# Optimization experiments

Measured on AMD Instinct MI355X. Metric: run time of the kernel, lower is better.

## Reference

```python
import jax, jax.numpy as jnp
import numpy as np

N, IN_F, OUT_F, R = 8192, 4096, 4096, 16
ALPHA = 32
SCALING = ALPHA / R  # 2.0


def setup_inputs() -> dict:
    key = jax.random.key(0)
    k1, k2, k3, k4, k5 = jax.random.split(key, 5)
    return {
        "x": jax.random.normal(k1, (N, IN_F), dtype=jnp.float32),
        "W": jax.random.normal(k2, (OUT_F, IN_F), dtype=jnp.float32) * 0.02,
        "b": jax.random.normal(k3, (OUT_F,), dtype=jnp.float32) * 0.02,
        "lora_A": jax.random.normal(k4, (R, IN_F), dtype=jnp.float32) * 0.02,
        "lora_B": jax.random.normal(k5, (OUT_F, R), dtype=jnp.float32) * 0.02,
    }


def reference(x, W, b, lora_A, lora_B):
    # Base linear: x [N, in_f] @ W.T [in_f, out_f] + b -> [N, out_f]
    result = jnp.einsum('ni,oi->no', x, W) + b
    # LoRA path: (B @ (A @ x.T)).T * scaling == (x @ A.T) @ B.T * scaling
    lora = jnp.einsum('nr,or->no', jnp.einsum('ni,ri->nr', x, lora_A), lora_B)
    return result + lora * SCALING
```

## Files before the change

### kernel.cpp

```cpp
#include <hip/hip_runtime.h>
#include <hip/hip_bf16.h>
#include <stdint.h>

#define N_ROWS 8192
#define IN_F   4096
#define OUT_F  4096
#define R_LORA 16
#define KP     4160

typedef __bf16 bf16_t;
typedef __attribute__((ext_vector_type(8))) __bf16 bf16x8;
typedef __attribute__((ext_vector_type(4))) __bf16 bf16x4;
typedef __attribute__((ext_vector_type(4))) float  f32x4;
typedef __attribute__((ext_vector_type(16))) float f32x16;

__device__ __forceinline__ void load16_lds(const bf16_t* g, bf16_t* l) {
    auto gp = (const __attribute__((address_space(1))) void*)g;
    auto lp = (__attribute__((address_space(3))) void*)(uint32_t)(uintptr_t)l;
    __builtin_amdgcn_global_load_lds(gp, lp, 16, 0, 0);
}

#define PREPA_BLOCKS 2048

__global__ __launch_bounds__(256) void prep_fused(const float* __restrict__ x,
                                                  const float* __restrict__ W,
                                                  const float* __restrict__ bias,
                                                  const float* __restrict__ lA,
                                                  const float* __restrict__ lB,
                                                  bf16_t* __restrict__ Aw,
                                                  bf16_t* __restrict__ Bw) {
    int b = blockIdx.x;
    int t = threadIdx.x;
    if (b < PREPA_BLOCKS) {
        int row0 = b * 4;
        for (int rr = 0; rr < 4; ++rr) {
            int row = row0 + rr;
            const float4* xr = (const float4*)(x + (size_t)row * IN_F);
            bf16_t* ar = Aw + (size_t)row * KP;
            for (int s = t; s < 512; s += 256) {
                float4 f0 = xr[2 * s];
                float4 f1 = xr[2 * s + 1];
                bf16x8 v;
                v[0] = (bf16_t)f0.x; v[1] = (bf16_t)f0.y;
                v[2] = (bf16_t)f0.z; v[3] = (bf16_t)f0.w;
                v[4] = (bf16_t)f1.x; v[5] = (bf16_t)f1.y;
                v[6] = (bf16_t)f1.z; v[7] = (bf16_t)f1.w;
                *(bf16x8*)(ar + s * 8) = v;
            }
            if (t < 64) ar[IN_F + t] = (t == 0) ? (bf16_t)1.0f : (bf16_t)0.0f;
        }
    } else {
        int o0 = (b - PREPA_BLOCKS) * 4;
        float bl[4][R_LORA];
        for (int oo = 0; oo < 4; ++oo)
            for (int r = 0; r < R_LORA; ++r)
                bl[oo][r] = 2.0f * lB[(o0 + oo) * R_LORA + r];

        for (int j = 0; j < IN_F / (256 * 4); ++j) {
            int i4 = (j * 256 + t) * 4;
            f32x4 acc[4];
            for (int oo = 0; oo < 4; ++oo) {
                float4 w = *(const float4*)(W + (size_t)(o0 + oo) * IN_F + i4);
                acc[oo] = (f32x4){w.x, w.y, w.z, w.w};
            }
            for (int r = 0; r < R_LORA; ++r) {
                float4 a = *(const float4*)(lA + (size_t)r * IN_F + i4);
                for (int oo = 0; oo < 4; ++oo) {
                    acc[oo][0] += bl[oo][r] * a.x;
                    acc[oo][1] += bl[oo][r] * a.y;
                    acc[oo][2] += bl[oo][r] * a.z;
                    acc[oo][3] += bl[oo][r] * a.w;
                }
            }
            for (int oo = 0; oo < 4; ++oo) {
                bf16x4 v;
                v[0] = (bf16_t)acc[oo][0]; v[1] = (bf16_t)acc[oo][1];
                v[2] = (bf16_t)acc[oo][2]; v[3] = (bf16_t)acc[oo][3];
                *(bf16x4*)(Bw + (size_t)(o0 + oo) * KP + i4) = v;
            }
        }
        {
            int oo = t >> 6;
            int c  = IN_F + (t & 63);
            float v = (c == IN_F) ? bias[o0 + oo] : 0.0f;
            Bw[(size_t)(o0 + oo) * KP + c] = (bf16_t)v;
        }
    }
}

#define BM 256
#define BN 256
#define BK 64
#define NT (KP / BK)

__global__ __launch_bounds__(512, 2) void gemm_bt(const bf16_t* __restrict__ A,
                                                  const bf16_t* __restrict__ B,
                                                  float* __restrict__ C) {
    __shared__ __align__(16) bf16_t lds[2][2][BM * BK];

    int bid = blockIdx.x;
    int swz = (bid & 7) * 64 + (bid >> 3);
    int bm  = swz & 31;
    int bn  = swz >> 5;
    int rowBase = bm * BM;
    int colBase = bn * BN;

    const int t    = threadIdx.x;
    const int lane = t & 63;
    const int wave = t >> 6;
    const int l31  = lane & 31;
    const int lhi  = lane >> 5;
    const int l7   = lane & 7;
    const int wr   = wave >> 2;
    const int wc   = wave & 3;

    int rowOffA[4], colOffB[2];
#pragma unroll
    for (int rf = 0; rf < 4; ++rf) rowOffA[rf] = (wr * 128 + rf * 32 + l31) * BK;
#pragma unroll
    for (int cf = 0; cf < 2; ++cf) colOffB[cf] = (wc * 64 + cf * 32 + l31) * BK;

    uint32_t srcA[4], srcB[4];
#pragma unroll
    for (int s = 0; s < 4; ++s) {
        int c = s * 512 + t;
        int r = c >> 3, p = c & 7;
        uint32_t off = (uint32_t)(r * KP + ((p ^ (r & 7)) << 3));
        srcA[s] = (uint32_t)(rowBase * KP) + off;
        srcB[s] = (uint32_t)(colBase * KP) + off;
    }

    auto stage = [&](int bsel, int k0) {
#pragma unroll
        for (int s = 0; s < 4; ++s)
            load16_lds(A + srcA[s] + k0, &lds[bsel][0][(s * 512 + t) * 8]);
#pragma unroll
        for (int s = 0; s < 4; ++s)
            load16_lds(B + srcB[s] + k0, &lds[bsel][1][(s * 512 + t) * 8]);
    };

    f32x16 acc[4][2];
#pragma unroll
    for (int rf = 0; rf < 4; ++rf)
#pragma unroll
        for (int cf = 0; cf < 2; ++cf)
#pragma unroll
            for (int r = 0; r < 16; ++r) acc[rf][cf][r] = 0.f;

#define COMPUTE(bsel)                                                          \
    do {                                                                       \
        const bf16_t* Ab = &lds[bsel][0][0];                                   \
        const bf16_t* Bb = &lds[bsel][1][0];                                   \
        _Pragma("unroll")                                                      \
        for (int ks = 0; ks < 4; ++ks) {                                       \
            int pos = ((((ks << 1) | lhi)) ^ l7) << 3;                         \
            bf16x8 af[4], bf[2];                                               \
            _Pragma("unroll")                                                  \
            for (int rf = 0; rf < 4; ++rf)                                     \
                af[rf] = *(const bf16x8*)&Ab[rowOffA[rf] + pos];               \
            _Pragma("unroll")                                                  \
            for (int cf = 0; cf < 2; ++cf)                                     \
                bf[cf] = *(const bf16x8*)&Bb[colOffB[cf] + pos];               \
            __builtin_amdgcn_s_setprio(1);                                     \
            _Pragma("unroll")                                                  \
            for (int rf = 0; rf < 4; ++rf)                                     \
                _Pragma("unroll")                                              \
                for (int cf = 0; cf < 2; ++cf)                                 \
                    acc[rf][cf] = __builtin_amdgcn_mfma_f32_32x32x16_bf16(     \
                        af[rf], bf[cf], acc[rf][cf], 0, 0, 0);                 \
            __builtin_amdgcn_s_setprio(0);                                     \
        }                                                                      \
    } while (0)

    stage(0, 0);

    for (int kt = 0; kt < NT - 1; ++kt) {
        const int cur = kt & 1;
        const int nb  = cur ^ 1;
        __builtin_amdgcn_s_barrier();
        stage(nb, (kt + 1) * BK);
        asm volatile("s_waitcnt vmcnt(8)" ::: "memory");
        __builtin_amdgcn_s_barrier();
        COMPUTE(cur);
    }
    {
        __builtin_amdgcn_s_barrier();
        asm volatile("s_waitcnt vmcnt(0)" ::: "memory");
        __builtin_amdgcn_s_barrier();
        COMPUTE(0);
    }
#undef COMPUTE

#pragma unroll
    for (int rf = 0; rf < 4; ++rf) {
        int rB = rowBase + wr * 128 + rf * 32 + 4 * lhi;
#pragma unroll
        for (int cf = 0; cf < 2; ++cf) {
            int col = colBase + wc * 64 + cf * 32 + l31;
#pragma unroll
            for (int reg = 0; reg < 16; ++reg) {
                int row = rB + (reg & 3) + 8 * (reg >> 2);
                C[(size_t)row * OUT_F + col] = acc[rf][cf][reg];
            }
        }
    }
}

extern "C" void kernel_launch(void* const* d_in, const int* in_sizes, int n_in,
                              void* d_out, int out_size, void* d_ws, size_t ws_size,
                              hipStream_t stream) {
    const float* x  = (const float*)d_in[0];
    const float* W  = (const float*)d_in[1];
    const float* b  = (const float*)d_in[2];
    const float* lA = (const float*)d_in[3];
    const float* lB = (const float*)d_in[4];
    float* out = (float*)d_out;

    bf16_t* Aw = (bf16_t*)d_ws;
    bf16_t* Bw = Aw + (size_t)N_ROWS * KP;

    prep_fused<<<PREPA_BLOCKS + OUT_F / 4, 256, 0, stream>>>(x, W, b, lA, lB, Aw, Bw);
    gemm_bt<<<(N_ROWS / BM) * (OUT_F / BN), 512, 0, stream>>>(Aw, Bw, out);
}
```

Baseline: 538.9 us.

## Restructure GEMM inner loop into quadrant-wise LDS reads interleaved with MFMA

Splits each K-tile's compute into four quadrant phases. Each phase reads one slice of A or B fragments from LDS for all four k-steps, then issues MFMAs, with block barriers between phases so waves stay in lockstep, ping-pong style. The loop is unified with the tail iteration, and the top-of-loop barrier is replaced by one at the end. This trades extra barriers and a redundant re-read of A quadrant 0 for fewer fragment registers live at once and better LDS/MFMA overlap across waves.

```diff
diff --git a/kernel.cpp b/kernel.cpp
--- a/kernel.cpp
+++ b/kernel.cpp
@@ -114,12 +114,6 @@
     const int wr   = wave >> 2;
     const int wc   = wave & 3;
 
-    int rowOffA[4], colOffB[2];
-#pragma unroll
-    for (int rf = 0; rf < 4; ++rf) rowOffA[rf] = (wr * 128 + rf * 32 + l31) * BK;
-#pragma unroll
-    for (int cf = 0; cf < 2; ++cf) colOffB[cf] = (wc * 64 + cf * 32 + l31) * BK;
-
     uint32_t srcA[4], srcB[4];
 #pragma unroll
     for (int s = 0; s < 4; ++s) {
@@ -147,49 +141,73 @@
 #pragma unroll
             for (int r = 0; r < 16; ++r) acc[rf][cf][r] = 0.f;
 
-#define COMPUTE(bsel)                                                          \
+    bf16x8 af[2][4];
+    bf16x8 bfr[4];
+
+#define READ_A(qr)                                                             \
     do {                                                                       \
-        const bf16_t* Ab = &lds[bsel][0][0];                                   \
-        const bf16_t* Bb = &lds[bsel][1][0];                                   \
+        _Pragma("unroll")                                                      \
+        for (int rf2 = 0; rf2 < 2; ++rf2)                                      \
+            _Pragma("unroll")                                                  \
+            for (int ks = 0; ks < 4; ++ks) {                                   \
+                int row = wr * 128 + (qr) * 64 + rf2 * 32 + l31;               \
+                int pos = ((((ks << 1) | lhi)) ^ l7) << 3;                     \
+                af[rf2][ks] = *(const bf16x8*)&Ab[row * BK + pos];             \
+            }                                                                  \
+    } while (0)
+
+#define READ_B(qc)                                                             \
+    do {                                                                       \
         _Pragma("unroll")                                                      \
         for (int ks = 0; ks < 4; ++ks) {                                       \
+            int col = wc * 64 + (qc) * 32 + l31;                               \
             int pos = ((((ks << 1) | lhi)) ^ l7) << 3;                         \
-            bf16x8 af[4], bf[2];                                               \
-            _Pragma("unroll")                                                  \
-            for (int rf = 0; rf < 4; ++rf)                                     \
-                af[rf] = *(const bf16x8*)&Ab[rowOffA[rf] + pos];               \
-            _Pragma("unroll")                                                  \
-            for (int cf = 0; cf < 2; ++cf)                                     \
-                bf[cf] = *(const bf16x8*)&Bb[colOffB[cf] + pos];               \
-            __builtin_amdgcn_s_setprio(1);                                     \
-            _Pragma("unroll")                                                  \
-            for (int rf = 0; rf < 4; ++rf)                                     \
-                _Pragma("unroll")                                              \
-                for (int cf = 0; cf < 2; ++cf)                                 \
-                    acc[rf][cf] = __builtin_amdgcn_mfma_f32_32x32x16_bf16(     \
-                        af[rf], bf[cf], acc[rf][cf], 0, 0, 0);                 \
-            __builtin_amdgcn_s_setprio(0);                                     \
+            bfr[ks] = *(const bf16x8*)&Bb[col * BK + pos];                     \
         }                                                                      \
     } while (0)
 
+#define MMA(qr, qc)                                                            \
+    do {                                                                       \
+        __builtin_amdgcn_s_setprio(1);                                         \
+        _Pragma("unroll")                                                      \
+        for (int ks = 0; ks < 4; ++ks)                                         \
+            _Pragma("unroll")                                                  \
+            for (int rf2 = 0; rf2 < 2; ++rf2)                                  \
+                acc[(qr) * 2 + rf2][qc] =                                      \
+                    __builtin_amdgcn_mfma_f32_32x32x16_bf16(                   \
+                        af[rf2][ks], bfr[ks], acc[(qr) * 2 + rf2][qc], 0, 0, 0);\
+        __builtin_amdgcn_s_setprio(0);                                         \
+    } while (0)
+
     stage(0, 0);
 
-    for (int kt = 0; kt < NT - 1; ++kt) {
+    for (int kt = 0; kt < NT; ++kt) {
         const int cur = kt & 1;
         const int nb  = cur ^ 1;
-        __builtin_amdgcn_s_barrier();
-        stage(nb, (kt + 1) * BK);
-        asm volatile("s_waitcnt vmcnt(8)" ::: "memory");
-        __builtin_amdgcn_s_barrier();
-        COMPUTE(cur);
-    }
-    {
-        __builtin_amdgcn_s_barrier();
-        asm volatile("s_waitcnt vmcnt(0)" ::: "memory");
-        __builtin_amdgcn_s_barrier();
-        COMPUTE(0);
-    }
-#undef COMPUTE
+        const bf16_t* Ab = &lds[cur][0][0];
+        const bf16_t* Bb = &lds[cur][1][0];
+
+        if (kt + 1 < NT) {
+            stage(nb, (kt + 1) * BK);
+            asm volatile("s_waitcnt vmcnt(8)" ::: "memory");
+        } else {
+            asm volatile("s_waitcnt vmcnt(0)" ::: "memory");
+        }
+        __builtin_amdgcn_s_barrier();
+
+        READ_A(0); READ_B(0); MMA(0, 0);
+        __builtin_amdgcn_s_barrier();
+        READ_A(1);            MMA(1, 0);
+        __builtin_amdgcn_s_barrier();
+        READ_B(1);            MMA(1, 1);
+        __builtin_amdgcn_s_barrier();
+        READ_A(0);            MMA(0, 1);
+        asm volatile("" ::: "memory");
+        __builtin_amdgcn_s_barrier();
+    }
+#undef READ_A
+#undef READ_B
+#undef MMA
 
 #pragma unroll
     for (int rf = 0; rf < 4; ++rf) {
```

After: 569.3 us. 5.6% more time.
